# Optimization experiments

Measured on AMD Instinct MI355X. Metric: run time of the kernel, lower is better.

The kernel has to match this reference:

```python
import jax, jax.numpy as jnp
import numpy as np

M, N, E, ES, D = 50000, 20000, 200000, 100000, 256

def _ln(x, g, b, eps=1e-5):
    mu = jnp.mean(x, -1, keepdims=True)
    var = jnp.mean((x - mu) ** 2, -1, keepdims=True)
    return (x - mu) * jax.lax.rsqrt(var + eps) * g + b

def _bn_train(x, g, b, eps=1e-5):
    # BatchNorm1d forward in training mode: batch statistics over rows
    mu = jnp.mean(x, 0)
    var = jnp.mean((x - mu) ** 2, 0)
    return (x - mu) * jax.lax.rsqrt(var + eps) * g + b

def _encoder(x, source, Wq, Wk, Wv, Wm, bm, ln1_g, ln1_b, mw1, mb1, mw2, mb2, ln2_g, ln2_b):
    # LoFTR-style linear-attention cross encoder, nhead=1
    Q = jax.nn.elu(x @ Wq) + 1.0          # [L,D]
    K = jax.nn.elu(source @ Wk) + 1.0     # [S,D]
    V = source @ Wv                        # [S,D]
    KV = K.T @ V                           # [D,D]
    Z = Q @ jnp.sum(K, 0) + 1e-6           # [L]
    msg = (Q @ KV) / Z[:, None]            # [L,D]
    msg = _ln(msg @ Wm + bm, ln1_g, ln1_b)
    y = jnp.concatenate([x, msg], -1)      # [L,2D]
    y = jax.nn.relu(y @ mw1 + mb1) @ mw2 + mb2
    return x + _ln(y, ln2_g, ln2_b)

def setup_inputs() -> dict:
    key = jax.random.key(0)
    ks = jax.random.split(key, 20)
    s = 1.0 / np.sqrt(D)
    s2 = 1.0 / np.sqrt(2 * D)
    inp = {
        'h_nodes': jax.random.normal(ks[0], (M, D), jnp.float32),
        's_u': jax.random.normal(ks[1], (N, D), jnp.float32),
        'g_src': jax.random.randint(ks[2], (E,), 0, M, jnp.int32),
        'g_dst': jax.random.randint(ks[3], (E,), 0, M, jnp.int32),
        's_src': jax.random.randint(ks[4], (ES,), 0, N, jnp.int32),
        's_dst': jax.random.randint(ks[5], (ES,), 0, N, jnp.int32),
        'conv_w': jax.random.normal(ks[6], (1, 2, 3), jnp.float32) * 0.3,
        'conv_b': jnp.zeros((1,), jnp.float32),
        'W2': jax.random.normal(ks[7], (D, D), jnp.float32) * s,
        'b2': jnp.zeros((D,), jnp.float32),
        'W4': jax.random.normal(ks[8], (D, D), jnp.float32) * s,
        'b4': jnp.zeros((D,), jnp.float32),
        'bn_g': jnp.ones((D,), jnp.float32),
        'bn_b': jnp.zeros((D,), jnp.float32),
        'Wq': jax.random.normal(ks[9], (D, D), jnp.float32) * s,
        'Wk': jax.random.normal(ks[10], (D, D), jnp.float32) * s,
        'Wv': jax.random.normal(ks[11], (D, D), jnp.float32) * s,
        'Wm': jax.random.normal(ks[12], (D, D), jnp.float32) * s,
        'bm': jnp.zeros((D,), jnp.float32),
        'ln1_g': jnp.ones((D,), jnp.float32),
        'ln1_b': jnp.zeros((D,), jnp.float32),
        'mw1': jax.random.normal(ks[13], (2 * D, 2 * D), jnp.float32) * s2,
        'mb1': jnp.zeros((2 * D,), jnp.float32),
        'mw2': jax.random.normal(ks[14], (2 * D, D), jnp.float32) * s2,
        'mb2': jnp.zeros((D,), jnp.float32),
        'ln2_g': jnp.ones((D,), jnp.float32),
        'ln2_b': jnp.zeros((D,), jnp.float32),
    }
    return inp

def reference(h_nodes, s_u, g_src, g_dst, s_src, s_dst, conv_w, conv_b, W2, b2, W4, b4,
              bn_g, bn_b, Wq, Wk, Wv, Wm, bm, ln1_g, ln1_b, mw1, mb1, mw2, mb2, ln2_g, ln2_b):
    enc = lambda x, src: _encoder(x, src, Wq, Wk, Wv, Wm, bm, ln1_g, ln1_b,
                                  mw1, mb1, mw2, mb2, ln2_g, ln2_b)
    # --- local edge features: gather src/dst, Conv1d(2->1,k=3,p=1), Linear ---
    src = h_nodes[g_src]                         # [E,D]
    dst = h_nodes[g_dst]                         # [E,D]
    edge_in = jnp.stack([src, dst], 1)           # [E,2,D]
    xp = jnp.pad(edge_in, ((0, 0), (0, 0), (1, 1)))
    conv = conv_b[0]
    for c in range(2):
        for j in range(3):
            conv = conv + conv_w[0, c, j] * xp[:, c, j:j + D]
    lr_e_local = conv @ W2 + b2                  # [E,D]
    # --- CrossTransformer (shared encoder weights across HUR/UVR/UUR) ---
    x = enc(h_nodes[:N], s_u)                    # user refinement [N,D]
    h_n = h_nodes.at[:N].set(x)
    edge = enc(h_n[g_src], h_n[g_dst])           # [E,D]
    social_edge = enc(x[s_src], x[s_dst])        # [ES,D]
    # --- fuse + BN + ReLU (dropout off for deterministic reference) ---
    lr_e = edge @ W4 + b4 + lr_e_local
    lr_e = jax.nn.relu(_bn_train(lr_e, bn_g, bn_b))
    social_edge = _bn_train(social_edge, bn_g, bn_b)
    return (lr_e, social_edge)
```

## Files before the change

### kernel.cpp

```cpp
#include <hip/hip_runtime.h>

static constexpr int Mn  = 50000;
static constexpr int Nn  = 20000;
static constexpr int En  = 200000;
static constexpr int ESn = 100000;

typedef short short8v __attribute__((ext_vector_type(8)));
typedef short short4v __attribute__((ext_vector_type(4)));
typedef float f32x4   __attribute__((ext_vector_type(4)));

__device__ __forceinline__ float b2f(unsigned short h) {
  unsigned int u = ((unsigned int)h) << 16;
  return __builtin_bit_cast(float, u);
}
__device__ __forceinline__ unsigned short f2b(float f) {
  unsigned int u = __builtin_bit_cast(unsigned int, f);
  u = (u + 0x7FFFu + ((u >> 16) & 1u)) >> 16;
  return (unsigned short)u;
}
__device__ __forceinline__ void gld16(const void* g, void* l) {
  __builtin_amdgcn_global_load_lds(
      (const __attribute__((address_space(1))) void*)g,
      (__attribute__((address_space(3))) void*)l, 16, 0, 0);
}

__global__ __launch_bounds__(256) void cvt_b(const float* __restrict__ s,
                                             unsigned short* __restrict__ d, long n) {
  long g  = (long)blockIdx.x*256 + threadIdx.x;
  long st = (long)gridDim.x*256;
  for (; g*8 < n; g += st) {
    const float4 a = *(const float4*)(s + g*8);
    const float4 b = *(const float4*)(s + g*8 + 4);
    short8v o;
    o[0]=(short)f2b(a.x); o[1]=(short)f2b(a.y); o[2]=(short)f2b(a.z); o[3]=(short)f2b(a.w);
    o[4]=(short)f2b(b.x); o[5]=(short)f2b(b.y); o[6]=(short)f2b(b.z); o[7]=(short)f2b(b.w);
    *(short8v*)(d + g*8) = o;
  }
}

__global__ __launch_bounds__(128) void wp_build(const float* __restrict__ W, int K, int N,
    unsigned short* __restrict__ WP, int KKd, int kg0) {
  const int t = threadIdx.x;
  const int kk2 = t >> 6, l = t & 63;
  const int c16 = blockIdx.x, ky = blockIdx.y;
  const int k0 = ky*64 + kk2*32 + (l>>4)*8;
  const int n  = c16*16 + (l&15);
  short8v o;
#pragma unroll
  for (int e=0;e<8;++e) o[e] = (short)f2b(W[(long)(k0+e)*N + n]);
  *(short8v*)(WP + (((long)c16*KKd + kg0 + ky*2+kk2)*64 + l)*8) = o;
}

__global__ __launch_bounds__(256) void kvw_mul(const float* __restrict__ KV,
    const float* __restrict__ Wm, float* __restrict__ KVW) {
  const int a = blockIdx.x;
  const int c = threadIdx.x;
  float s = 0.f;
  for (int b = 0; b < 256; ++b) s += KV[a*256 + b] * Wm[(long)b*256 + c];
  KVW[a*256 + c] = s;
}

__global__ __launch_bounds__(256) void count_idx(const int* __restrict__ idx, int n,
                                                 int* __restrict__ cnt) {
  int i = blockIdx.x*256 + threadIdx.x;
  const int st = gridDim.x*256;
  for (; i < n; i += st) atomicAdd(&cnt[idx[i]], 1);
}

__global__ __launch_bounds__(256,3) void gemm_kv(
    const unsigned short* __restrict__ X, int aoff,
    const unsigned short* __restrict__ WkP, const unsigned short* __restrict__ WvP,
    unsigned short* __restrict__ KbT, unsigned short* __restrict__ VbT,
    float* __restrict__ pS, int ldp, int nrows, const int* __restrict__ cntw)
{
  __shared__ short xb[4][64*64];
  const int t = threadIdx.x;
  const int w = t >> 6, l = t & 63, q = l >> 4, hw = l & 15;
  const int r0 = blockIdx.x << 6;

  {
    const int sr = l >> 3, sc = l & 7;
    const int gcol = ((sc ^ sr) << 3);
#pragma unroll
    for (int j=0;j<2;++j) {
      int lr = r0 + j*32 + w*8 + sr;
      int lrc = lr < nrows ? lr : nrows-1;
      const unsigned short* src = X + (long)(aoff+lrc)*256 + gcol;
#pragma unroll
      for (int ks=0;ks<4;++ks)
        gld16(src + ks*64, &xb[ks][(j*32 + w*8)*64]);
    }
  }
  asm volatile("s_waitcnt vmcnt(0)" ::: "memory");
  __builtin_amdgcn_s_barrier();

#pragma unroll
  for (int pass=0; pass<2; ++pass) {
    const unsigned short* WP = pass ? WvP : WkP;
    unsigned short* O = pass ? VbT : KbT;
    f32x4 acc[4][4];
#pragma unroll
    for (int m=0;m<4;++m)
#pragma unroll
      for (int n=0;n<4;++n) acc[m][n] = (f32x4){0.f,0.f,0.f,0.f};
    short8v bfc[4], bfn[4];
#pragma unroll
    for (int n=0;n<4;++n)
      bfc[n] = *(const short8v*)(WP + (((long)(w*4+n)*8)*64 + l)*8);
#pragma unroll
    for (int st=0; st<8; ++st) {
      if (st < 7) {
#pragma unroll
        for (int n=0;n<4;++n)
          bfn[n] = *(const short8v*)(WP + (((long)(w*4+n)*8 + st+1)*64 + l)*8);
      }
      const int ks = st >> 1;
      const int kc = ((st&1)<<2) + q;
      short8v af[4];
#pragma unroll
      for (int m=0;m<4;++m)
        af[m] = *(const short8v*)&xb[ks][(m*16+hw)*64 + ((kc^(hw&7))<<3)];
      __builtin_amdgcn_s_setprio(1);
#pragma unroll
      for (int m=0;m<4;++m)
#pragma unroll
        for (int n=0;n<4;++n)
          acc[m][n] = __builtin_amdgcn_mfma_f32_16x16x32_bf16(af[m], bfc[n], acc[m][n], 0,0,0);
      __builtin_amdgcn_s_setprio(0);
#pragma unroll
      for (int n=0;n<4;++n) bfc[n] = bfn[n];
    }
    float colsum[4] = {0.f,0.f,0.f,0.f};
#pragma unroll
    for (int m=0;m<4;++m)
#pragma unroll
      for (int n=0;n<4;++n) {
        const int c = w*64 + n*16 + hw;
        short4v o4;
#pragma unroll
        for (int i=0;i<4;++i) {
          const int lr = r0 + m*16 + q*4 + i;
          float v = 0.f;
          if (lr < nrows) {
            v = acc[m][n][i];
            if (pass == 0) {
              v = v > 0.f ? v + 1.f : __expf(v);
              if (cntw) v *= (float)cntw[aoff + lr];
            }
          }
          if (pass == 0) colsum[n] += v;
          o4[i] = (short)f2b(v);
        }
        *(short4v*)(O + (long)c*ldp + r0 + m*16 + q*4) = o4;
      }
    if (pass == 0) {
#pragma unroll
      for (int n=0;n<4;++n) {
        float s = colsum[n];
        s += __shfl_xor(s, 16);
        s += __shfl_xor(s, 32);
        if (q == 0) pS[(long)blockIdx.x*256 + w*64 + n*16 + hw] = s;
      }
    }
  }
}

__global__ __launch_bounds__(256) void ksum_red(const float* __restrict__ pS, int nb,
    float* __restrict__ Ks) {
  __shared__ float ws[4];
  const int c = blockIdx.x;
  const int t = threadIdx.x;
  float s = 0.f;
  for (int b = t; b < nb; b += 256) s += pS[(long)b*256 + c];
#pragma unroll
  for (int off=32; off; off>>=1) s += __shfl_xor(s, off);
  if ((t & 63) == 0) ws[t >> 6] = s;
  __syncthreads();
  if (t == 0) Ks[c] += ws[0] + ws[1] + ws[2] + ws[3];
}

__global__ __launch_bounds__(256,4) void ktv_mfma(
    const unsigned short* __restrict__ KbT, const unsigned short* __restrict__ VbT,
    int ldp, int rpp, float* __restrict__ pKV)
{
  const int t  = threadIdx.x;
  const int w  = t >> 6;
  const int l  = t & 63;
  const int q  = l >> 4;
  const int hw = l & 15;
  const int wa = w >> 1, wb = w & 1;
  const int a0 = blockIdx.x << 7;
  const int b0 = blockIdx.y << 7;
  const int rbeg = blockIdx.z * rpp;
  const int rend = min(ldp, rbeg + rpp);

  f32x4 acc[4][4];
#pragma unroll
  for (int m=0;m<4;++m)
#pragma unroll
    for (int n=0;n<4;++n) acc[m][n] = (f32x4){0.f,0.f,0.f,0.f};

  const unsigned short* ap[4];
  const unsigned short* bp[4];
#pragma unroll
  for (int m=0;m<4;++m) ap[m] = KbT + (long)(a0 + wa*64 + m*16 + hw)*ldp + q*8;
#pragma unroll
  for (int n=0;n<4;++n) bp[n] = VbT + (long)(b0 + wb*64 + n*16 + hw)*ldp + q*8;

#pragma unroll 4
  for (int r = rbeg; r < rend; r += 32) {
    short8v af[4], bf[4];
#pragma unroll
    for (int m=0;m<4;++m) af[m] = *(const short8v*)(ap[m] + r);
#pragma unroll
    for (int n=0;n<4;++n) bf[n] = *(const short8v*)(bp[n] + r);
#pragma unroll
    for (int m=0;m<4;++m)
#pragma unroll
      for (int n=0;n<4;++n)
        acc[m][n] = __builtin_amdgcn_mfma_f32_16x16x32_bf16(af[m], bf[n], acc[m][n], 0,0,0);
  }

  const long base = (long)blockIdx.z * 65536;
#pragma unroll
  for (int m=0;m<4;++m)
#pragma unroll
    for (int i=0;i<4;++i) {
      const int a = a0 + wa*64 + m*16 + q*4 + i;
#pragma unroll
      for (int n=0;n<4;++n) {
        const int b = b0 + wb*64 + n*16 + hw;
        pKV[base + (long)a*256 + b] = acc[m][n][i];
      }
    }
}

__global__ __launch_bounds__(256) void kv_accum(const float* __restrict__ pKV, int P,
                                                float* __restrict__ KV) {
  const int i = blockIdx.x*256 + threadIdx.x;
  float s = 0.f;
  for (int p=0;p<P;++p) s += pKV[(long)p*65536 + i];
  KV[i] += s;
}

template<int OMODE>
__global__ __launch_bounds__(256,2) void encB(
    const unsigned short* __restrict__ X, int aoff,
    const unsigned short* __restrict__ WqP, const unsigned short* __restrict__ KVWP,
    const unsigned short* __restrict__ m1P, const unsigned short* __restrict__ m2P,
    const float* __restrict__ Ksum, const float* __restrict__ bmv,
    const float* __restrict__ l1g, const float* __restrict__ l1b,
    const float* __restrict__ mb1, const float* __restrict__ mb2,
    const float* __restrict__ l2g, const float* __restrict__ l2b,
    const unsigned short* __restrict__ WfP,
    void* outv, int dc0, int nrows)
{
  __shared__ short xb[4][64*64];
  __shared__ short qb[4][64*64];
  __shared__ short y1b[64*64];
  __shared__ float2 red[64][4];
  __shared__ float Zl[64];

  const int t = threadIdx.x;
  const int w = t >> 6, l = t & 63, q = l >> 4, hw = l & 15;
  const int wc = w;
  const int r0 = blockIdx.x << 6;
  const int sr = l >> 3, sc = l & 7;
  const int gcol = ((sc ^ sr) << 3);

  {
#pragma unroll
    for (int j=0;j<2;++j) {
      int lr = r0 + j*32 + w*8 + sr;
      int lrc = lr < nrows ? lr : nrows-1;
      const unsigned short* src = X + (long)(aoff+lrc)*256 + gcol;
#pragma unroll
      for (int ks=0;ks<4;++ks)
        gld16(src + ks*64, &xb[ks][(j*32 + w*8)*64]);
    }
  }
  asm volatile("s_waitcnt vmcnt(0)" ::: "memory");
  __builtin_amdgcn_s_barrier();

  f32x4 acc[4][4];

  auto GEMM256 = [&](const short* Asrc, const unsigned short* WP) {
#pragma unroll
    for (int m=0;m<4;++m)
#pragma unroll
      for (int n=0;n<4;++n) acc[m][n] = (f32x4){0.f,0.f,0.f,0.f};
    short8v bfc[4], bfn[4];
#pragma unroll
    for (int n=0;n<4;++n)
      bfc[n] = *(const short8v*)(WP + (((long)(wc*4+n)*8)*64 + l)*8);
#pragma unroll
    for (int st=0; st<8; ++st) {
      if (st < 7) {
#pragma unroll
        for (int n=0;n<4;++n)
          bfn[n] = *(const short8v*)(WP + (((long)(wc*4+n)*8 + st+1)*64 + l)*8);
      }
      const int ks = st >> 1;
      const int kc = ((st&1)<<2) + q;
      short8v af[4];
#pragma unroll
      for (int m=0;m<4;++m)
        af[m] = *(const short8v*)&Asrc[ks*4096 + (m*16+hw)*64 + ((kc^(hw&7))<<3)];
      __builtin_amdgcn_s_setprio(1);
#pragma unroll
      for (int m=0;m<4;++m)
#pragma unroll
        for (int n=0;n<4;++n)
          acc[m][n] = __builtin_amdgcn_mfma_f32_16x16x32_bf16(af[m], bfc[n], acc[m][n], 0,0,0);
      __builtin_amdgcn_s_setprio(0);
#pragma unroll
      for (int n=0;n<4;++n) bfc[n] = bfn[n];
    }
  };

  GEMM256(&xb[0][0], WqP);
  {
    float ksv[4];
#pragma unroll
    for (int n=0;n<4;++n) ksv[n] = Ksum[wc*64+n*16+hw];
#pragma unroll
    for (int m=0;m<4;++m)
#pragma unroll
      for (int n=0;n<4;++n)
#pragma unroll
        for (int i=0;i<4;++i) {
          float v = acc[m][n][i];
          acc[m][n][i] = v > 0.f ? v + 1.f : __expf(v);
        }
#pragma unroll
    for (int m=0;m<4;++m)
#pragma unroll
      for (int i=0;i<4;++i) {
        float z = 0.f;
#pragma unroll
        for (int n=0;n<4;++n) z += acc[m][n][i]*ksv[n];
#pragma unroll
        for (int off=1; off<16; off<<=1) z += __shfl_xor(z, off);
        if (hw==0) red[m*16+q*4+i][wc] = make_float2(z, 0.f);
      }
#pragma unroll
    for (int m=0;m<4;++m)
#pragma unroll
      for (int i=0;i<4;++i) {
        const int row = m*16+q*4+i;
        const int sw = row & 7;
#pragma unroll
        for (int n=0;n<4;++n)
          qb[wc][row*64 + (((n*2+(hw>>3)) ^ sw)<<3) + (hw&7)] = (short)f2b(acc[m][n][i]);
      }
  }
  __syncthreads();
  if (wc==0 && hw==0) {
#pragma unroll
    for (int m=0;m<4;++m)
#pragma unroll
      for (int i=0;i<4;++i) {
        const int row = m*16+q*4+i;
        Zl[row] = red[row][0].x + red[row][1].x + red[row][2].x + red[row][3].x + 1e-6f;
      }
  }

  GEMM256(&qb[0][0], KVWP);
  __syncthreads();
#pragma unroll
  for (int m=0;m<4;++m) {
    const f32x4 z = *(const f32x4*)&Zl[m*16+q*4];
#pragma unroll
    for (int i=0;i<4;++i) {
      const float iz = 1.f / z[i];
#pragma unroll
      for (int n=0;n<4;++n) acc[m][n][i] *= iz;
    }
  }
  {
    float lg[4], lb[4];
#pragma unroll
    for (int n=0;n<4;++n) {
      const int c = wc*64+n*16+hw;
      const float bv = bmv[c];
      lg[n] = l1g[c]; lb[n] = l1b[c];
#pragma unroll
      for (int m=0;m<4;++m)
#pragma unroll
        for (int i=0;i<4;++i) acc[m][n][i] += bv;
    }
    float s1[4][4], s2[4][4];
#pragma unroll
    for (int m=0;m<4;++m)
#pragma unroll
      for (int i=0;i<4;++i) {
        float s=0.f, sq=0.f;
#pragma unroll
        for (int n=0;n<4;++n){ const float v=acc[m][n][i]; s+=v; sq+=v*v; }
        s1[m][i]=s; s2[m][i]=sq;
      }
#pragma unroll
    for (int off=1; off<16; off<<=1)
#pragma unroll
      for (int m=0;m<4;++m)
#pragma unroll
        for (int i=0;i<4;++i) {
          s1[m][i] += __shfl_xor(s1[m][i], off);
          s2[m][i] += __shfl_xor(s2[m][i], off);
        }
    if (hw==0) {
#pragma unroll
      for (int m=0;m<4;++m)
#pragma unroll
        for (int i=0;i<4;++i)
          red[m*16+q*4+i][wc] = make_float2(s1[m][i], s2[m][i]);
    }
    __syncthreads();
#pragma unroll
    for (int m=0;m<4;++m)
#pragma unroll
      for (int i=0;i<4;++i) {
        const int row = m*16+q*4+i;
        float ts=0.f, tq=0.f;
#pragma unroll
        for (int ww=0;ww<4;++ww){ const float2 v=red[row][ww]; ts+=v.x; tq+=v.y; }
        const float mmu = ts*(1.f/256.f);
        float var = tq*(1.f/256.f) - mmu*mmu;
        var = var>0.f ? var : 0.f;
        const float rs = rsqrtf(var + 1e-5f);
        const int sw = row & 7;
#pragma unroll
        for (int n=0;n<4;++n) {
          const float v = (acc[m][n][i]-mmu)*rs*lg[n] + lb[n];
          qb[wc][row*64 + (((n*2+(hw>>3)) ^ sw)<<3) + (hw&7)] = (short)f2b(v);
        }
      }
  }
  __syncthreads();

  f32x4 oacc[4][4];
#pragma unroll
  for (int m=0;m<4;++m)
#pragma unroll
    for (int n=0;n<4;++n) oacc[m][n] = (f32x4){0.f,0.f,0.f,0.f};

  for (int ct=0; ct<8; ++ct) {
    f32x4 ya[4];
#pragma unroll
    for (int m=0;m<4;++m) ya[m] = (f32x4){0.f,0.f,0.f,0.f};
    {
      short8v b0c, b0n;
      b0c = *(const short8v*)(m1P + (((long)(ct*4+wc)*16)*64 + l)*8);
#pragma unroll
      for (int st=0; st<16; ++st) {
        if (st < 15)
          b0n = *(const short8v*)(m1P + (((long)(ct*4+wc)*16 + st+1)*64 + l)*8);
        const int ks = st >> 1;
        const int kc = ((st&1)<<2) + q;
        const short* As_ = (ks<4) ? &xb[ks][0] : &qb[ks-4][0];
        __builtin_amdgcn_s_setprio(1);
#pragma unroll
        for (int m=0;m<4;++m) {
          const short8v af = *(const short8v*)&As_[(m*16+hw)*64 + ((kc^(hw&7))<<3)];
          ya[m] = __builtin_amdgcn_mfma_f32_16x16x32_bf16(af, b0c, ya[m], 0,0,0);
        }
        __builtin_amdgcn_s_setprio(0);
        b0c = b0n;
      }
    }
    const float b1 = mb1[ct*64 + wc*16 + hw];
#pragma unroll
    for (int m=0;m<4;++m)
#pragma unroll
      for (int i=0;i<4;++i) {
        const int row = m*16+q*4+i;
        float v = ya[m][i] + b1; v = v>0.f ? v : 0.f;
        y1b[row*64 + (((wc*2+(hw>>3)) ^ (row&7))<<3) + (hw&7)] = (short)f2b(v);
      }
    __syncthreads();
    {
      short8v bfc[4], bfn[4];
#pragma unroll
      for (int n=0;n<4;++n)
        bfc[n] = *(const short8v*)(m2P + (((long)(wc*4+n)*16 + ct*2)*64 + l)*8);
#pragma unroll
      for (int kk=0;kk<2;++kk) {
        if (kk == 0) {
#pragma unroll
          for (int n=0;n<4;++n)
            bfn[n] = *(const short8v*)(m2P + (((long)(wc*4+n)*16 + ct*2+1)*64 + l)*8);
        }
        const int kc = (kk<<2)+q;
        short8v af[4];
#pragma unroll
        for (int m=0;m<4;++m)
          af[m] = *(const short8v*)&y1b[(m*16+hw)*64 + ((kc^(hw&7))<<3)];
        __builtin_amdgcn_s_setprio(1);
#pragma unroll
        for (int m=0;m<4;++m)
#pragma unroll
          for (int n=0;n<4;++n)
            oacc[m][n] = __builtin_amdgcn_mfma_f32_16x16x32_bf16(af[m], bfc[n], oacc[m][n], 0,0,0);
        __builtin_amdgcn_s_setprio(0);
#pragma unroll
        for (int n=0;n<4;++n) bfc[n] = bfn[n];
      }
    }
    __syncthreads();
  }

  {
    float lg[4], lb[4];
#pragma unroll
    for (int n=0;n<4;++n) {
      const int c = wc*64+n*16+hw;
      const float bv = mb2[c];
      lg[n] = l2g[c]; lb[n] = l2b[c];
#pragma unroll
      for (int m=0;m<4;++m)
#pragma unroll
        for (int i=0;i<4;++i) oacc[m][n][i] += bv;
    }
    float s1[4][4], s2[4][4];
#pragma unroll
    for (int m=0;m<4;++m)
#pragma unroll
      for (int i=0;i<4;++i) {
        float s=0.f, sq=0.f;
#pragma unroll
        for (int n=0;n<4;++n){ const float v=oacc[m][n][i]; s+=v; sq+=v*v; }
        s1[m][i]=s; s2[m][i]=sq;
      }
#pragma unroll
    for (int off=1; off<16; off<<=1)
#pragma unroll
      for (int m=0;m<4;++m)
#pragma unroll
        for (int i=0;i<4;++i) {
          s1[m][i] += __shfl_xor(s1[m][i], off);
          s2[m][i] += __shfl_xor(s2[m][i], off);
        }
    if (hw==0) {
#pragma unroll
      for (int m=0;m<4;++m)
#pragma unroll
        for (int i=0;i<4;++i)
          red[m*16+q*4+i][wc] = make_float2(s1[m][i], s2[m][i]);
    }
    __syncthreads();
#pragma unroll
    for (int m=0;m<4;++m)
#pragma unroll
      for (int i=0;i<4;++i) {
        const int row = m*16+q*4+i;
        const int lr = r0 + row;
        if (lr >= nrows) continue;
        float ts=0.f, tq=0.f;
#pragma unroll
        for (int ww=0;ww<4;++ww){ const float2 v=red[row][ww]; ts+=v.x; tq+=v.y; }
        const float mmu = ts*(1.f/256.f);
        float var = tq*(1.f/256.f) - mmu*mmu;
        var = var>0.f ? var : 0.f;
        const float rs = rsqrtf(var + 1e-5f);
        const int sw = row & 7;
#pragma unroll
        for (int n=0;n<4;++n) {
          const int c = wc*64+n*16+hw;
          float v = (oacc[m][n][i]-mmu)*rs*lg[n] + lb[n];
          v += b2f((unsigned short)xb[wc][row*64 + (((n*2+(hw>>3)) ^ sw)<<3) + (hw&7)]);
          if constexpr (OMODE == 2) {
            qb[wc][row*64 + (((n*2+(hw>>3)) ^ sw)<<3) + (hw&7)] = (short)f2b(v);
          } else {
            const long off2 = (long)(dc0+lr)*256 + c;
            if constexpr (OMODE == 1) ((float*)outv)[off2] = v;
            else ((unsigned short*)outv)[off2] = f2b(v);
          }
        }
      }
  }

  if constexpr (OMODE == 2) {
    __syncthreads();
    GEMM256(&qb[0][0], WfP);
#pragma unroll
    for (int m=0;m<4;++m)
#pragma unroll
      for (int i=0;i<4;++i) {
        const int lr = r0 + m*16 + q*4 + i;
        if (lr >= nrows) continue;
#pragma unroll
        for (int n=0;n<4;++n)
          ((float*)outv)[(long)(dc0+lr)*256 + wc*64+n*16+hw] = acc[m][n][i];
      }
  }
}

__global__ __launch_bounds__(256,3) void edge_final(
    const float* __restrict__ h, const int* __restrict__ gs, const int* __restrict__ gd,
    const float* __restrict__ cw, const float* __restrict__ cb,
    const unsigned short* __restrict__ W2P, const float* __restrict__ EW4,
    const float* __restrict__ b4, const float* __restrict__ b2,
    float* __restrict__ lr_e, float* __restrict__ pstat, int nrows)
{
  __shared__ short xb[4][64*64];
  const int t = threadIdx.x;
  const int w = t >> 6, l = t & 63, q = l >> 4, hw = l & 15;
  const int r0 = blockIdx.x << 6;

  const float c0=cw[0],c1=cw[1],c2=cw[2],c3=cw[3],c4=cw[4],c5=cw[5],cbb=cb[0];
  for (int it=0; it<16; ++it) {
    const int row = w*16 + it;
    const int lr = r0 + row;
    const int lrc = lr < nrows ? lr : nrows-1;
    const float4 s = *(const float4*)(h + (long)gs[lrc]*256 + l*4);
    const float4 d = *(const float4*)(h + (long)gd[lrc]*256 + l*4);
    float smw = __shfl_up(s.w, 1); if (l==0) smw = 0.f;
    float spx = __shfl_down(s.x, 1); if (l==63) spx = 0.f;
    float dmw = __shfl_up(d.w, 1); if (l==0) dmw = 0.f;
    float dpx = __shfl_down(d.x, 1); if (l==63) dpx = 0.f;
    short4v o;
    o[0]=(short)f2b(cbb + c0*smw + c1*s.x + c2*s.y + c3*dmw + c4*d.x + c5*d.y);
    o[1]=(short)f2b(cbb + c0*s.x + c1*s.y + c2*s.z + c3*d.x + c4*d.y + c5*d.z);
    o[2]=(short)f2b(cbb + c0*s.y + c1*s.z + c2*s.w + c3*d.y + c4*d.z + c5*d.w);
    o[3]=(short)f2b(cbb + c0*s.z + c1*s.w + c2*spx + c3*d.z + c4*d.w + c5*dpx);
    const int ks = l >> 4;
    const int g  = (l & 15) >> 1;
    *(short4v*)&xb[ks][row*64 + ((g ^ (row&7))<<3) + (l&1)*4] = o;
  }
  __syncthreads();

  f32x4 acc[4][4];
#pragma unroll
  for (int m=0;m<4;++m)
#pragma unroll
    for (int n=0;n<4;++n) acc[m][n] = (f32x4){0.f,0.f,0.f,0.f};
  short8v bfc[4], bfn[4];
#pragma unroll
  for (int n=0;n<4;++n)
    bfc[n] = *(const short8v*)(W2P + (((long)(w*4+n)*8)*64 + l)*8);
#pragma unroll
  for (int st=0; st<8; ++st) {
    if (st < 7) {
#pragma unroll
      for (int n=0;n<4;++n)
        bfn[n] = *(const short8v*)(W2P + (((long)(w*4+n)*8 + st+1)*64 + l)*8);
    }
    const int ks = st >> 1;
    const int kc = ((st&1)<<2) + q;
    short8v af[4];
#pragma unroll
    for (int m=0;m<4;++m)
      af[m] = *(const short8v*)&xb[ks][(m*16+hw)*64 + ((kc^(hw&7))<<3)];
    __builtin_amdgcn_s_setprio(1);
#pragma unroll
    for (int m=0;m<4;++m)
#pragma unroll
      for (int n=0;n<4;++n)
        acc[m][n] = __builtin_amdgcn_mfma_f32_16x16x32_bf16(af[m], bfc[n], acc[m][n], 0,0,0);
    __builtin_amdgcn_s_setprio(0);
#pragma unroll
    for (int n=0;n<4;++n) bfc[n] = bfn[n];
  }
  float bia[4];
#pragma unroll
  for (int n=0;n<4;++n) {
    const int c = w*64+n*16+hw;
    bia[n] = b4[c] + b2[c];
  }
  float cs[4] = {0.f,0.f,0.f,0.f};
  float cq2[4] = {0.f,0.f,0.f,0.f};
#pragma unroll
  for (int m=0;m<4;++m)
#pragma unroll
    for (int i=0;i<4;++i) {
      const int lr = r0 + m*16 + q*4 + i;
      if (lr >= nrows) continue;
      const long rid = (long)gs[lr];
#pragma unroll
      for (int n=0;n<4;++n) {
        const int c = w*64+n*16+hw;
        const float v = acc[m][n][i] + EW4[rid*256 + c] + bia[n];
        cs[n] += v; cq2[n] += v*v;
        lr_e[(long)lr*256 + c] = v;
      }
    }
#pragma unroll
  for (int n=0;n<4;++n) {
    float a = cs[n];
    a += __shfl_xor(a, 16);
    a += __shfl_xor(a, 32);
    float b = cq2[n];
    b += __shfl_xor(b, 16);
    b += __shfl_xor(b, 32);
    if (q == 0) {
      const int c = w*64+n*16+hw;
      pstat[(long)blockIdx.x*512 + c] = a;
      pstat[(long)blockIdx.x*512 + 256 + c] = b;
    }
  }
}

template<bool R>
__global__ __launch_bounds__(256) void bn_apply(float* __restrict__ X, long rows,
    const float* __restrict__ sc, const float* __restrict__ sh) {
  const long n4 = rows*64;
  long i = (long)blockIdx.x*256 + threadIdx.x;
  const long st = (long)gridDim.x*256;
  for (; i<n4; i+=st) {
    const int cq = (int)(i & 63);
    float4 v = ((float4*)X)[i];
    const float4 s4 = ((const float4*)sc)[cq];
    const float4 h4 = ((const float4*)sh)[cq];
    v.x = v.x*s4.x + h4.x; v.y = v.y*s4.y + h4.y;
    v.z = v.z*s4.z + h4.z; v.w = v.w*s4.w + h4.w;
    if (R) { v.x=fmaxf(v.x,0.f); v.y=fmaxf(v.y,0.f); v.z=fmaxf(v.z,0.f); v.w=fmaxf(v.w,0.f); }
    ((float4*)X)[i] = v;
  }
}

__global__ __launch_bounds__(256) void bnw_stats(const float* __restrict__ X,
    const int* __restrict__ cnt, int rows, float* __restrict__ part) {
  const int b = blockIdx.x, c = threadIdx.x;
  float s=0.f, s2=0.f;
  for (int r=b; r<rows; r+=64) {
    const float wgt = (float)cnt[r];
    if (wgt != 0.f) {
      const float v = X[(long)r*256 + c];
      s += wgt*v; s2 += wgt*v*v;
    }
  }
  part[(long)b*512 + c] = s;
  part[(long)b*512 + 256 + c] = s2;
}

__global__ __launch_bounds__(256) void bn_mid(const float* __restrict__ part, int PE,
    float* __restrict__ mid) {
  const int g = blockIdx.x, c = threadIdx.x;
  float s=0.f, s2=0.f;
  for (int p=g; p<PE; p+=64) {
    s  += part[(long)p*512 + c];
    s2 += part[(long)p*512 + 256 + c];
  }
  mid[(long)g*512 + c] = s;
  mid[(long)g*512 + 256 + c] = s2;
}

__global__ __launch_bounds__(256) void bn_finalize(const float* __restrict__ part, int P,
    long rows, const float* __restrict__ g, const float* __restrict__ b,
    float* __restrict__ scale, float* __restrict__ shift) {
  const int c = threadIdx.x;
  float s=0.f, s2=0.f;
  for (int p=0;p<P;++p) { s += part[(long)p*512 + c]; s2 += part[(long)p*512 + 256 + c]; }
  const float inv = 1.f/(float)rows;
  const float mu = s*inv;
  float var = s2*inv - mu*mu;
  var = var > 0.f ? var : 0.f;
  const float rs = rsqrtf(var + 1e-5f);
  scale[c] = g[c]*rs;
  shift[c] = b[c] - mu*g[c]*rs;
}

__global__ __launch_bounds__(256) void bn_apply_gather(const float* __restrict__ nodeS,
    const int* __restrict__ sidx, long rows,
    const float* __restrict__ sc, const float* __restrict__ sh,
    float* __restrict__ out) {
  const long n4 = rows*64;
  long i = (long)blockIdx.x*256 + threadIdx.x;
  const long st = (long)gridDim.x*256;
  for (; i<n4; i+=st) {
    const long row = i >> 6;
    const int cq = (int)(i & 63);
    const long rid = (long)sidx[row];
    float4 v = *(const float4*)(nodeS + rid*256 + cq*4);
    const float4 s4 = ((const float4*)sc)[cq];
    const float4 h4 = ((const float4*)sh)[cq];
    v.x = v.x*s4.x + h4.x; v.y = v.y*s4.y + h4.y;
    v.z = v.z*s4.z + h4.z; v.w = v.w*s4.w + h4.w;
    ((float4*)out)[i] = v;
  }
}

struct Ctx {
  const unsigned short *WkP,*WvP,*WqP,*m1P,*m2P;
  unsigned short* KVWP;
  const float *Wm;
  float* KVW;
  const float *bm,*l1g,*l1b,*mb1,*mb2,*l2g,*l2b;
  unsigned short *bufA,*bufB;
  float *pKV,*pS,*KV;
  long CH;
  hipStream_t st;
};

static void phaseA(const Ctx& c, long S, const unsigned short* Bsrc, const int* cnt) {
  hipMemsetAsync(c.KV, 0, 65792*sizeof(float), c.st);
  for (long s0=0; s0<S; s0+=c.CH) {
    const int n = (int)((S-s0 < c.CH) ? (S-s0) : c.CH);
    const int gb = (n+63)/64;
    const int ldp = gb*64;
    gemm_kv<<<gb,256,0,c.st>>>(Bsrc, (int)s0, c.WkP, c.WvP, c.bufA, c.bufB, c.pS, ldp, n, cnt);
    const int P = (ldp+511)/512;
    ktv_mfma<<<dim3(2,2,P),256,0,c.st>>>(c.bufA, c.bufB, ldp, 512, c.pKV);
    kv_accum<<<256,256,0,c.st>>>(c.pKV, P, c.KV);
    ksum_red<<<256,256,0,c.st>>>(c.pS, gb, c.KV+65536);
  }
  kvw_mul<<<256,256,0,c.st>>>(c.KV, c.Wm, c.KVW);
  wp_build<<<dim3(16,4),128,0,c.st>>>(c.KVW, 256, 256, c.KVWP, 8, 0);
}

template<int OMODE>
static void phaseB(const Ctx& c, long L, const unsigned short* Asrc, void* out,
                   const unsigned short* WfP) {
  const float* Ksum = c.KV + 65536;
  for (long l0=0; l0<L; l0+=c.CH) {
    const int n = (int)((L-l0 < c.CH) ? (L-l0) : c.CH);
    const int gb = (n+63)/64;
    encB<OMODE><<<gb,256,0,c.st>>>(Asrc, (int)l0,
        c.WqP, c.KVWP, c.m1P, c.m2P, Ksum, c.bm, c.l1g, c.l1b,
        c.mb1, c.mb2, c.l2g, c.l2b, WfP, out, (int)l0, n);
  }
}

extern "C" void kernel_launch(void* const* d_in, const int* in_sizes, int n_in,
                              void* d_out, int out_size, void* d_ws, size_t ws_size,
                              hipStream_t stream) {
  const float* h_nodes = (const float*)d_in[0];
  const float* s_u     = (const float*)d_in[1];
  const int*   g_src   = (const int*)d_in[2];
  const int*   g_dst   = (const int*)d_in[3];
  const int*   s_src   = (const int*)d_in[4];
  const int*   s_dst   = (const int*)d_in[5];
  const float* conv_w  = (const float*)d_in[6];
  const float* conv_b  = (const float*)d_in[7];
  const float* W2      = (const float*)d_in[8];
  const float* b2      = (const float*)d_in[9];
  const float* W4      = (const float*)d_in[10];
  const float* b4      = (const float*)d_in[11];
  const float* bn_g    = (const float*)d_in[12];
  const float* bn_b    = (const float*)d_in[13];
  const float* Wq      = (const float*)d_in[14];
  const float* Wk      = (const float*)d_in[15];
  const float* Wv      = (const float*)d_in[16];
  const float* Wm      = (const float*)d_in[17];
  const float* bm      = (const float*)d_in[18];
  const float* l1g     = (const float*)d_in[19];
  const float* l1b     = (const float*)d_in[20];
  const float* mw1     = (const float*)d_in[21];
  const float* mb1     = (const float*)d_in[22];
  const float* mw2     = (const float*)d_in[23];
  const float* mb2     = (const float*)d_in[24];
  const float* l2g     = (const float*)d_in[25];
  const float* l2b     = (const float*)d_in[26];
  (void)in_sizes; (void)n_in; (void)out_size;

  float* lr_e = (float*)d_out;
  float* soc  = lr_e + (size_t)En*256;

  char* base = (char*)d_ws;
  size_t off = 0;
  auto carve = [&](size_t bytes)->void* {
    void* p = (void*)(base + off);
    off = (off + bytes + 255) & ~(size_t)255;
    return p;
  };
  unsigned short* h_nb = (unsigned short*)carve((size_t)Mn*256*2);
  unsigned short* s_ub = (unsigned short*)carve((size_t)Nn*256*2);
  unsigned short* WkP  = (unsigned short*)carve(65536*2);
  unsigned short* WvP  = (unsigned short*)carve(65536*2);
  unsigned short* WqP  = (unsigned short*)carve(65536*2);
  unsigned short* m1P  = (unsigned short*)carve(262144*2);
  unsigned short* m2P  = (unsigned short*)carve(131072*2);
  unsigned short* W4P  = (unsigned short*)carve(65536*2);
  unsigned short* W2P  = (unsigned short*)carve(65536*2);
  unsigned short* KVWP = (unsigned short*)carve(65536*2);
  float* KV            = (float*)carve(65792*4);
  float* KVW           = (float*)carve(65536*4);
  float* bnpart        = (float*)carve((size_t)3200*512*4);
  float* bnmid         = (float*)carve((size_t)64*512*4);
  float* bnscale       = (float*)carve(256*4);
  float* bnshift       = (float*)carve(256*4);
  float* EW4           = (float*)carve((size_t)Mn*256*4);
  float* nodeS         = (float*)carve((size_t)Nn*256*4);
  int* cntg            = (int*)carve((size_t)Mn*4);
  int* cnts            = (int*)carve((size_t)Nn*4);
  int* cntss           = (int*)carve((size_t)Nn*4);

  const size_t remain = ws_size > off ? ws_size - off : 0;
  long CH = (long)(remain / 1589248) * 1024;
  if (CH > 65536) CH = 65536;
  if (CH < 2048)  CH = 2048;
  unsigned short* bufA = (unsigned short*)carve((size_t)CH*256*2);
  unsigned short* bufB = (unsigned short*)carve((size_t)CH*256*2);
  float* pKV           = (float*)carve((size_t)((CH+511)/512)*65536*4);
  float* pS            = (float*)carve((size_t)(CH/64)*256*4);

  cvt_b<<<2048,256,0,stream>>>(h_nodes, h_nb, (long)Mn*256);
  cvt_b<<<1024,256,0,stream>>>(s_u, s_ub, (long)Nn*256);
  wp_build<<<dim3(16,4),128,0,stream>>>(Wk, 256,256, WkP, 8, 0);
  wp_build<<<dim3(16,4),128,0,stream>>>(Wv, 256,256, WvP, 8, 0);
  wp_build<<<dim3(16,4),128,0,stream>>>(Wq, 256,256, WqP, 8, 0);
  wp_build<<<dim3(32,8),128,0,stream>>>(mw1, 512,512, m1P, 16, 0);
  wp_build<<<dim3(16,8),128,0,stream>>>(mw2, 512,256, m2P, 16, 0);
  wp_build<<<dim3(16,4),128,0,stream>>>(W4, 256,256, W4P, 8, 0);
  wp_build<<<dim3(16,4),128,0,stream>>>(W2, 256,256, W2P, 8, 0);
  hipMemsetAsync(cntg, 0, (size_t)Mn*4, stream);
  hipMemsetAsync(cnts, 0, (size_t)Nn*4, stream);
  hipMemsetAsync(cntss,0, (size_t)Nn*4, stream);
  count_idx<<<512,256,0,stream>>>(g_dst, En, cntg);
  count_idx<<<512,256,0,stream>>>(s_dst, ESn, cnts);
  count_idx<<<512,256,0,stream>>>(s_src, ESn, cntss);

  Ctx c;
  c.WkP=WkP; c.WvP=WvP; c.WqP=WqP; c.m1P=m1P; c.m2P=m2P;
  c.KVWP=KVWP; c.Wm=Wm; c.KVW=KVW;
  c.bm=bm; c.l1g=l1g; c.l1b=l1b; c.mb1=mb1; c.mb2=mb2; c.l2g=l2g; c.l2b=l2b;
  c.bufA=bufA; c.bufB=bufB;
  c.pKV=pKV; c.pS=pS; c.KV=KV;
  c.CH=CH; c.st=stream;

  phaseA(c, Nn, s_ub, nullptr);
  phaseB<0>(c, Nn, h_nb, h_nb, nullptr);

  phaseA(c, Mn, h_nb, cntg);
  phaseB<2>(c, Mn, h_nb, EW4, W4P);
  {
    const int gbE = (En+63)/64;
    edge_final<<<gbE,256,0,stream>>>(h_nodes, g_src, g_dst, conv_w, conv_b,
                                     W2P, EW4, b4, b2, lr_e, bnpart, En);
    bn_mid<<<64,256,0,stream>>>(bnpart, gbE, bnmid);
    bn_finalize<<<1,256,0,stream>>>(bnmid, 64, (long)En, bn_g, bn_b, bnscale, bnshift);
    bn_apply<true><<<2048,256,0,stream>>>(lr_e, (long)En, bnscale, bnshift);
  }

  phaseA(c, Nn, h_nb, cnts);
  phaseB<1>(c, Nn, h_nb, nodeS, nullptr);
  bnw_stats<<<64,256,0,stream>>>(nodeS, cntss, Nn, bnmid);
  bn_finalize<<<1,256,0,stream>>>(bnmid, 64, (long)ESn, bn_g, bn_b, bnscale, bnshift);
  bn_apply_gather<<<2048,256,0,stream>>>(nodeS, s_src, (long)ESn, bnscale, bnshift, soc);
}
```

Before: 1.135 ms.

## Split encB 64-row tile across eight waves to halve per-wave accumulators

New measurement: 1.169 ms. +3.1%, slower.

```diff
diff --git a/kernel.cpp b/kernel.cpp
--- a/kernel.cpp
+++ b/kernel.cpp
@@ -244,7 +244,7 @@
 }
 
 template<int OMODE>
-__global__ __launch_bounds__(256,2) void encB(
+__global__ __launch_bounds__(512,4) void encB(
     const unsigned short* __restrict__ X, int aoff,
     const unsigned short* __restrict__ WqP, const unsigned short* __restrict__ KVWP,
     const unsigned short* __restrict__ m1P, const unsigned short* __restrict__ m2P,
@@ -263,30 +263,28 @@
 
   const int t = threadIdx.x;
   const int w = t >> 6, l = t & 63, q = l >> 4, hw = l & 15;
-  const int wc = w;
+  const int wc = w & 3, wr = w >> 2;
+  const int rb = wr * 32;
   const int r0 = blockIdx.x << 6;
   const int sr = l >> 3, sc = l & 7;
   const int gcol = ((sc ^ sr) << 3);
 
   {
-#pragma unroll
-    for (int j=0;j<2;++j) {
-      int lr = r0 + j*32 + w*8 + sr;
-      int lrc = lr < nrows ? lr : nrows-1;
-      const unsigned short* src = X + (long)(aoff+lrc)*256 + gcol;
-#pragma unroll
-      for (int ks=0;ks<4;++ks)
-        gld16(src + ks*64, &xb[ks][(j*32 + w*8)*64]);
-    }
+    int lr = r0 + w*8 + sr;
+    int lrc = lr < nrows ? lr : nrows-1;
+    const unsigned short* src = X + (long)(aoff+lrc)*256 + gcol;
+#pragma unroll
+    for (int ks=0;ks<4;++ks)
+      gld16(src + ks*64, &xb[ks][(w*8 + sr)*64]);
   }
   asm volatile("s_waitcnt vmcnt(0)" ::: "memory");
   __builtin_amdgcn_s_barrier();
 
-  f32x4 acc[4][4];
+  f32x4 acc[2][4];
 
   auto GEMM256 = [&](const short* Asrc, const unsigned short* WP) {
 #pragma unroll
-    for (int m=0;m<4;++m)
+    for (int m=0;m<2;++m)
 #pragma unroll
       for (int n=0;n<4;++n) acc[m][n] = (f32x4){0.f,0.f,0.f,0.f};
     short8v bfc[4], bfn[4];
@@ -302,13 +300,13 @@
       }
       const int ks = st >> 1;
       const int kc = ((st&1)<<2) + q;
-      short8v af[4];
-#pragma unroll
-      for (int m=0;m<4;++m)
-        af[m] = *(const short8v*)&Asrc[ks*4096 + (m*16+hw)*64 + ((kc^(hw&7))<<3)];
+      short8v af[2];
+#pragma unroll
+      for (int m=0;m<2;++m)
+        af[m] = *(const short8v*)&Asrc[ks*4096 + (rb + m*16+hw)*64 + ((kc^(hw&7))<<3)];
       __builtin_amdgcn_s_setprio(1);
 #pragma unroll
-      for (int m=0;m<4;++m)
+      for (int m=0;m<2;++m)
 #pragma unroll
         for (int n=0;n<4;++n)
           acc[m][n] = __builtin_amdgcn_mfma_f32_16x16x32_bf16(af[m], bfc[n], acc[m][n], 0,0,0);
@@ -324,7 +322,7 @@
 #pragma unroll
     for (int n=0;n<4;++n) ksv[n] = Ksum[wc*64+n*16+hw];
 #pragma unroll
-    for (int m=0;m<4;++m)
+    for (int m=0;m<2;++m)
 #pragma unroll
       for (int n=0;n<4;++n)
 #pragma unroll
@@ -333,7 +331,7 @@
           acc[m][n][i] = v > 0.f ? v + 1.f : __expf(v);
         }
 #pragma unroll
-    for (int m=0;m<4;++m)
+    for (int m=0;m<2;++m)
 #pragma unroll
       for (int i=0;i<4;++i) {
         float z = 0.f;
@@ -341,13 +339,13 @@
         for (int n=0;n<4;++n) z += acc[m][n][i]*ksv[n];
 #pragma unroll
         for (int off=1; off<16; off<<=1) z += __shfl_xor(z, off);
-        if (hw==0) red[m*16+q*4+i][wc] = make_float2(z, 0.f);
-      }
-#pragma unroll
-    for (int m=0;m<4;++m)
+        if (hw==0) red[rb + m*16+q*4+i][wc] = make_float2(z, 0.f);
+      }
+#pragma unroll
+    for (int m=0;m<2;++m)
 #pragma unroll
       for (int i=0;i<4;++i) {
-        const int row = m*16+q*4+i;
+        const int row = rb + m*16+q*4+i;
         const int sw = row & 7;
 #pragma unroll
         for (int n=0;n<4;++n)
@@ -357,10 +355,10 @@
   __syncthreads();
   if (wc==0 && hw==0) {
 #pragma unroll
-    for (int m=0;m<4;++m)
+    for (int m=0;m<2;++m)
 #pragma unroll
       for (int i=0;i<4;++i) {
-        const int row = m*16+q*4+i;
+        const int row = rb + m*16+q*4+i;
         Zl[row] = red[row][0].x + red[row][1].x + red[row][2].x + red[row][3].x + 1e-6f;
       }
   }
@@ -368,8 +366,8 @@
   GEMM256(&qb[0][0], KVWP);
   __syncthreads();
 #pragma unroll
-  for (int m=0;m<4;++m) {
-    const f32x4 z = *(const f32x4*)&Zl[m*16+q*4];
+  for (int m=0;m<2;++m) {
+    const f32x4 z = *(const f32x4*)&Zl[rb + m*16+q*4];
 #pragma unroll
     for (int i=0;i<4;++i) {
       const float iz = 1.f / z[i];
@@ -385,13 +383,13 @@
       const float bv = bmv[c];
       lg[n] = l1g[c]; lb[n] = l1b[c];
 #pragma unroll
-      for (int m=0;m<4;++m)
+      for (int m=0;m<2;++m)
 #pragma unroll
         for (int i=0;i<4;++i) acc[m][n][i] += bv;
     }
-    float s1[4][4], s2[4][4];
-#pragma unroll
-    for (int m=0;m<4;++m)
+    float s1[2][4], s2[2][4];
+#pragma unroll
+    for (int m=0;m<2;++m)
 #pragma unroll
       for (int i=0;i<4;++i) {
         float s=0.f, sq=0.f;
@@ -402,7 +400,7 @@
 #pragma unroll
     for (int off=1; off<16; off<<=1)
 #pragma unroll
-      for (int m=0;m<4;++m)
+      for (int m=0;m<2;++m)
 #pragma unroll
         for (int i=0;i<4;++i) {
           s1[m][i] += __shfl_xor(s1[m][i], off);
@@ -410,17 +408,17 @@
         }
     if (hw==0) {
 #pragma unroll
-      for (int m=0;m<4;++m)
+      for (int m=0;m<2;++m)
 #pragma unroll
         for (int i=0;i<4;++i)
-          red[m*16+q*4+i][wc] = make_float2(s1[m][i], s2[m][i]);
+          red[rb + m*16+q*4+i][wc] = make_float2(s1[m][i], s2[m][i]);
     }
     __syncthreads();
 #pragma unroll
-    for (int m=0;m<4;++m)
+    for (int m=0;m<2;++m)
 #pragma unroll
       for (int i=0;i<4;++i) {
-        const int row = m*16+q*4+i;
+        const int row = rb + m*16+q*4+i;
         float ts=0.f, tq=0.f;
 #pragma unroll
         for (int ww=0;ww<4;++ww){ const float2 v=red[row][ww]; ts+=v.x; tq+=v.y; }
@@ -438,16 +436,16 @@
   }
   __syncthreads();
 
-  f32x4 oacc[4][4];
-#pragma unroll
-  for (int m=0;m<4;++m)
+  f32x4 oacc[2][4];
+#pragma unroll
+  for (int m=0;m<2;++m)
 #pragma unroll
     for (int n=0;n<4;++n) oacc[m][n] = (f32x4){0.f,0.f,0.f,0.f};
 
   for (int ct=0; ct<8; ++ct) {
-    f32x4 ya[4];
-#pragma unroll
-    for (int m=0;m<4;++m) ya[m] = (f32x4){0.f,0.f,0.f,0.f};
+    f32x4 ya[2];
+#pragma unroll
+    for (int m=0;m<2;++m) ya[m] = (f32x4){0.f,0.f,0.f,0.f};
     {
       short8v b0c, b0n;
       b0c = *(const short8v*)(m1P + (((long)(ct*4+wc)*16)*64 + l)*8);
@@ -460,8 +458,8 @@
         const short* As_ = (ks<4) ? &xb[ks][0] : &qb[ks-4][0];
         __builtin_amdgcn_s_setprio(1);
 #pragma unroll
-        for (int m=0;m<4;++m) {
-          const short8v af = *(const short8v*)&As_[(m*16+hw)*64 + ((kc^(hw&7))<<3)];
+        for (int m=0;m<2;++m) {
+          const short8v af = *(const short8v*)&As_[(rb + m*16+hw)*64 + ((kc^(hw&7))<<3)];
           ya[m] = __builtin_amdgcn_mfma_f32_16x16x32_bf16(af, b0c, ya[m], 0,0,0);
         }
         __builtin_amdgcn_s_setprio(0);
@@ -470,10 +468,10 @@
     }
     const float b1 = mb1[ct*64 + wc*16 + hw];
 #pragma unroll
-    for (int m=0;m<4;++m)
+    for (int m=0;m<2;++m)
 #pragma unroll
       for (int i=0;i<4;++i) {
-        const int row = m*16+q*4+i;
+        const int row = rb + m*16+q*4+i;
         float v = ya[m][i] + b1; v = v>0.f ? v : 0.f;
         y1b[row*64 + (((wc*2+(hw>>3)) ^ (row&7))<<3) + (hw&7)] = (short)f2b(v);
       }
@@ -491,13 +489,13 @@
             bfn[n] = *(const short8v*)(m2P + (((long)(wc*4+n)*16 + ct*2+1)*64 + l)*8);
         }
         const int kc = (kk<<2)+q;
-        short8v af[4];
-#pragma unroll
-        for (int m=0;m<4;++m)
-          af[m] = *(const short8v*)&y1b[(m*16+hw)*64 + ((kc^(hw&7))<<3)];
+        short8v af[2];
+#pragma unroll
+        for (int m=0;m<2;++m)
+          af[m] = *(const short8v*)&y1b[(rb + m*16+hw)*64 + ((kc^(hw&7))<<3)];
         __builtin_amdgcn_s_setprio(1);
 #pragma unroll
-        for (int m=0;m<4;++m)
+        for (int m=0;m<2;++m)
 #pragma unroll
           for (int n=0;n<4;++n)
             oacc[m][n] = __builtin_amdgcn_mfma_f32_16x16x32_bf16(af[m], bfc[n], oacc[m][n], 0,0,0);
@@ -517,13 +515,13 @@
       const float bv = mb2[c];
       lg[n] = l2g[c]; lb[n] = l2b[c];
 #pragma unroll
-      for (int m=0;m<4;++m)
+      for (int m=0;m<2;++m)
 #pragma unroll
         for (int i=0;i<4;++i) oacc[m][n][i] += bv;
     }
-    float s1[4][4], s2[4][4];
-#pragma unroll
-    for (int m=0;m<4;++m)
+    float s1[2][4], s2[2][4];
+#pragma unroll
+    for (int m=0;m<2;++m)
 #pragma unroll
       for (int i=0;i<4;++i) {
         float s=0.f, sq=0.f;
@@ -534,7 +532,7 @@
 #pragma unroll
     for (int off=1; off<16; off<<=1)
 #pragma unroll
-      for (int m=0;m<4;++m)
+      for (int m=0;m<2;++m)
 #pragma unroll
         for (int i=0;i<4;++i) {
           s1[m][i] += __shfl_xor(s1[m][i], off);
@@ -542,17 +540,17 @@
         }
     if (hw==0) {
 #pragma unroll
-      for (int m=0;m<4;++m)
+      for (int m=0;m<2;++m)
 #pragma unroll
         for (int i=0;i<4;++i)
-          red[m*16+q*4+i][wc] = make_float2(s1[m][i], s2[m][i]);
+          red[rb + m*16+q*4+i][wc] = make_float2(s1[m][i], s2[m][i]);
     }
     __syncthreads();
 #pragma unroll
-    for (int m=0;m<4;++m)
+    for (int m=0;m<2;++m)
 #pragma unroll
       for (int i=0;i<4;++i) {
-        const int row = m*16+q*4+i;
+        const int row = rb + m*16+q*4+i;
         const int lr = r0 + row;
         if (lr >= nrows) continue;
         float ts=0.f, tq=0.f;
@@ -583,10 +581,10 @@
     __syncthreads();
     GEMM256(&qb[0][0], WfP);
 #pragma unroll
-    for (int m=0;m<4;++m)
+    for (int m=0;m<2;++m)
 #pragma unroll
       for (int i=0;i<4;++i) {
-        const int lr = r0 + m*16 + q*4 + i;
+        const int lr = r0 + rb + m*16 + q*4 + i;
         if (lr >= nrows) continue;
 #pragma unroll
         for (int n=0;n<4;++n)
@@ -815,7 +813,7 @@
   for (long l0=0; l0<L; l0+=c.CH) {
     const int n = (int)((L-l0 < c.CH) ? (L-l0) : c.CH);
     const int gb = (n+63)/64;
-    encB<OMODE><<<gb,256,0,c.st>>>(Asrc, (int)l0,
+    encB<OMODE><<<gb,512,0,c.st>>>(Asrc, (int)l0,
         c.WqP, c.KVWP, c.m1P, c.m2P, Ksum, c.bm, c.l1g, c.l1b,
         c.mb1, c.mb2, c.l2g, c.l2b, WfP, out, (int)l0, n);
   }
```
